# Kernel tuning notes

Hardware: AMD Instinct MI355X
Metric: run time of the kernel (lower is better)

## Reference

```python
import jax, jax.numpy as jnp
import numpy as np

N = 50000      # nodes
E = 800000     # edges (before self loops)
G = 64         # graphs in batch
F_IN = 11
HID = 64
C = 8
NEG_SLOPE = 0.2


def setup_inputs() -> dict:
    key = jax.random.key(0)
    ks = jax.random.split(key, 20)
    inp = {
        "x": jax.random.normal(ks[0], (N, F_IN), dtype=jnp.float32),
        "edge_index": jax.random.randint(ks[1], (2, E), 0, N, dtype=jnp.int64),
        "edge_attr": jax.random.normal(ks[2], (E, 17), dtype=jnp.float32),
        "batch": jnp.sort(jax.random.randint(ks[3], (N,), 0, G, dtype=jnp.int64)),
    }
    def glorot(k, shape):
        fan_in, fan_out = shape[0], shape[-1]
        s = jnp.sqrt(6.0 / (fan_in + fan_out))
        return jax.random.uniform(k, shape, jnp.float32, -s, s)
    # GATConv layers (heads=1): W [in,out], att vectors a_src/a_dst [out], bias [out]
    inp["W1"] = glorot(ks[4], (F_IN, HID)); inp["a1s"] = glorot(ks[5], (HID,)); inp["a1d"] = glorot(ks[6], (HID,)); inp["b1"] = jnp.zeros((HID,), jnp.float32)
    inp["W2"] = glorot(ks[7], (HID, HID)); inp["a2s"] = glorot(ks[8], (HID,)); inp["a2d"] = glorot(ks[9], (HID,)); inp["b2"] = jnp.zeros((HID,), jnp.float32)
    inp["W3"] = glorot(ks[10], (HID, C)); inp["a3s"] = glorot(ks[11], (C,)); inp["a3d"] = glorot(ks[12], (C,)); inp["b3"] = jnp.zeros((C,), jnp.float32)
    return inp


def _gat_layer(x, src, dst, W, a_s, a_d, b):
    # x: [N,in] -> h: [N,out]; single head, concat irrelevant for heads=1
    h = x @ W
    alpha_src = h @ a_s            # [N]
    alpha_dst = h @ a_d            # [N]
    e = jax.nn.leaky_relu(alpha_src[src] + alpha_dst[dst], negative_slope=NEG_SLOPE)  # [E']
    # segment-wise (per destination node) softmax over incoming edges
    m = jax.ops.segment_max(e, dst, num_segments=N)
    ex = jnp.exp(e - m[dst])
    denom = jax.ops.segment_sum(ex, dst, num_segments=N)
    alpha = ex / denom[dst]
    out = jax.ops.segment_sum(alpha[:, None] * h[src], dst, num_segments=N)
    return out + b


def reference(x, edge_index, edge_attr, batch, W1, a1s, a1d, b1, W2, a2s, a2d, b2, W3, a3s, a3d, b3):
    del edge_attr  # GATConv without edge_dim ignores edge_attr
    loop = jnp.arange(N, dtype=edge_index.dtype)
    src = jnp.concatenate([edge_index[0], loop])  # add self loops
    dst = jnp.concatenate([edge_index[1], loop])
    h = jax.nn.relu(_gat_layer(x, src, dst, W1, a1s, a1d, b1))
    h = jax.nn.relu(_gat_layer(h, src, dst, W2, a2s, a2d, b2))
    h = jax.nn.relu(_gat_layer(h, src, dst, W3, a3s, a3d, b3))
    # global mean pool over graphs
    counts = jax.ops.segment_sum(jnp.ones((N,), h.dtype), batch, num_segments=G)
    pooled = jax.ops.segment_sum(h, batch, num_segments=G) / jnp.maximum(counts, 1.0)[:, None]
    # dropout is identity in eval mode
    return jax.nn.sigmoid(pooled)
```

## Files before the change

kernel.cpp:

```cpp
#include <hip/hip_runtime.h>

#define NN 50000
#define EE 800000
#define GG 64
#define CC 8

#define NBKT 196
#define NCHK 782
#define CHUNK 1024
#define CAP 8192

__device__ unsigned g_done = 0;

__device__ __forceinline__ float lrelu(float z) { return fmaxf(z, 0.2f * z); }
__device__ __forceinline__ unsigned short f2bf(float v) {
    unsigned u = __float_as_uint(v);
    return (unsigned short)((u + 0x7FFFu + ((u >> 16) & 1u)) >> 16);
}
__device__ __forceinline__ float bf2f(unsigned short b) {
    return __uint_as_float(((unsigned)b) << 16);
}


__global__ __launch_bounds__(256) void k0_mm11_hist(const float* __restrict__ x, const float* __restrict__ W,
                                                    const float* __restrict__ avs, const float* __restrict__ avd,
                                                    unsigned short* __restrict__ h, float* __restrict__ as_,
                                                    float* __restrict__ ad_, const int* __restrict__ dst,
                                                    int* __restrict__ G) {
    __shared__ float xT[11 * 68];
    __shared__ float Wl[11 * 64];
    __shared__ float avl[64], adl[64];
    __shared__ int hist[NBKT];
    int t = threadIdx.x;
    int nbase = blockIdx.x * 64;
    for (int idx = t; idx < 11 * 64; idx += 256) Wl[idx] = W[idx];
    if (t < 64) { avl[t] = avs[t]; adl[t] = avd[t]; }
    for (int idx = t; idx < 64 * 11; idx += 256) {
        int n = idx / 11, k = idx - n * 11;
        int gn = nbase + n;
        if (gn >= NN) gn = NN - 1;
        xT[k * 68 + n] = x[gn * 11 + k];
    }
    for (int i = t; i < NBKT; i += 256) hist[i] = 0;
    __syncthreads();
    int f0 = (t & 15) * 4;
    int n0 = (t >> 4) * 4;
    float a00=0,a01=0,a02=0,a03=0, a10=0,a11=0,a12=0,a13=0;
    float a20=0,a21=0,a22=0,a23=0, a30=0,a31=0,a32=0,a33=0;
#pragma unroll
    for (int k = 0; k < 11; k++) {
        float4 xv = *(const float4*)&xT[k * 68 + n0];
        float4 wv = *(const float4*)&Wl[k * 64 + f0];
        a00 += xv.x * wv.x; a01 += xv.x * wv.y; a02 += xv.x * wv.z; a03 += xv.x * wv.w;
        a10 += xv.y * wv.x; a11 += xv.y * wv.y; a12 += xv.y * wv.z; a13 += xv.y * wv.w;
        a20 += xv.z * wv.x; a21 += xv.z * wv.y; a22 += xv.z * wv.z; a23 += xv.z * wv.w;
        a30 += xv.w * wv.x; a31 += xv.w * wv.y; a32 += xv.w * wv.z; a33 += xv.w * wv.w;
    }
    float4 av = *(const float4*)&avl[f0];
    float4 dv = *(const float4*)&adl[f0];
    float vs[4], vd[4];
    vs[0] = a00*av.x + a01*av.y + a02*av.z + a03*av.w;
    vs[1] = a10*av.x + a11*av.y + a12*av.z + a13*av.w;
    vs[2] = a20*av.x + a21*av.y + a22*av.z + a23*av.w;
    vs[3] = a30*av.x + a31*av.y + a32*av.z + a33*av.w;
    vd[0] = a00*dv.x + a01*dv.y + a02*dv.z + a03*dv.w;
    vd[1] = a10*dv.x + a11*dv.y + a12*dv.z + a13*dv.w;
    vd[2] = a20*dv.x + a21*dv.y + a22*dv.z + a23*dv.w;
    vd[3] = a30*dv.x + a31*dv.y + a32*dv.z + a33*dv.w;
#pragma unroll
    for (int o = 1; o < 16; o <<= 1) {
#pragma unroll
        for (int ni = 0; ni < 4; ni++) {
            vs[ni] += __shfl_xor(vs[ni], o);
            vd[ni] += __shfl_xor(vd[ni], o);
        }
    }
    ushort4* h4 = (ushort4*)h;
    int nn0 = nbase + n0;
    float rows[4][4] = {{a00,a01,a02,a03},{a10,a11,a12,a13},{a20,a21,a22,a23},{a30,a31,a32,a33}};
#pragma unroll
    for (int ni = 0; ni < 4; ni++) {
        if (nn0 + ni < NN) {
            ushort4 pv;
            pv.x = f2bf(rows[ni][0]); pv.y = f2bf(rows[ni][1]);
            pv.z = f2bf(rows[ni][2]); pv.w = f2bf(rows[ni][3]);
            h4[(nn0 + ni) * 16 + (t & 15)] = pv;
            if ((t & 15) == 0) { as_[nn0 + ni] = vs[ni]; ad_[nn0 + ni] = vd[ni]; }
        }
    }
    int e0 = blockIdx.x * CHUNK;
    int e1 = min(e0 + CHUNK, EE);
    for (int e = e0 + t; e < e1; e += 256) atomicAdd(&hist[dst[e] >> 8], 1);
    __syncthreads();
    for (int i = t; i < NBKT; i += 256) G[blockIdx.x * NBKT + i] = hist[i];
}


__global__ __launch_bounds__(256) void k1_scan(const int* __restrict__ G, int* __restrict__ offs,
                                               int* __restrict__ bT, float* __restrict__ pool,
                                               float* __restrict__ cntf, int* __restrict__ rowptr) {
    __shared__ int s[256];
    int t = threadIdx.x, j = blockIdx.x;
    int c0 = t * 4;
    int v0 = (c0 + 0 < NCHK) ? G[(c0 + 0) * NBKT + j] : 0;
    int v1 = (c0 + 1 < NCHK) ? G[(c0 + 1) * NBKT + j] : 0;
    int v2 = (c0 + 2 < NCHK) ? G[(c0 + 2) * NBKT + j] : 0;
    int v3 = (c0 + 3 < NCHK) ? G[(c0 + 3) * NBKT + j] : 0;
    int tsum = v0 + v1 + v2 + v3;
    s[t] = tsum;
    __syncthreads();
#pragma unroll
    for (int off = 1; off < 256; off <<= 1) {
        int u = (t >= off) ? s[t - off] : 0;
        __syncthreads();
        s[t] += u;
        __syncthreads();
    }
    int excl = s[t] - tsum;
    if (c0 + 0 < NCHK) offs[(c0 + 0) * NBKT + j] = excl;
    if (c0 + 1 < NCHK) offs[(c0 + 1) * NBKT + j] = excl + v0;
    if (c0 + 2 < NCHK) offs[(c0 + 2) * NBKT + j] = excl + v0 + v1;
    if (c0 + 3 < NCHK) offs[(c0 + 3) * NBKT + j] = excl + v0 + v1 + v2;
    if (t == 255) bT[j] = s[255];
    if (j == 0) {
        for (int i = t; i < GG * CC; i += 256) pool[i] = 0.f;
        if (t < GG) cntf[t] = 0.f;
        if (t == 0) rowptr[NN] = EE;
    }
}


__global__ __launch_bounds__(256) void k2_part(const int* __restrict__ src, const int* __restrict__ dst,
                                               const int* __restrict__ offs, const int* __restrict__ bT,
                                               unsigned* __restrict__ pairs) {
    __shared__ int s[256];
    __shared__ int bst[NBKT];
    __shared__ int cur[NBKT];
    int t = threadIdx.x, c = blockIdx.x;
    int v = (t < NBKT) ? bT[t] : 0;
    s[t] = v;
    __syncthreads();
#pragma unroll
    for (int off = 1; off < 256; off <<= 1) {
        int u = (t >= off) ? s[t - off] : 0;
        __syncthreads();
        s[t] += u;
        __syncthreads();
    }
    if (t < NBKT) bst[t] = s[t] - v;
    __syncthreads();
    for (int i = t; i < NBKT; i += 256) cur[i] = bst[i] + offs[c * NBKT + i];
    __syncthreads();
    int e0 = c * CHUNK, e1 = min(e0 + CHUNK, EE);
    for (int e = e0 + t; e < e1; e += 256) {
        int d = dst[e];
        int pos = atomicAdd(&cur[d >> 8], 1);
        pairs[pos] = (unsigned)src[e] | ((unsigned)(d & 255) << 16);
    }
}


__global__ __launch_bounds__(256) void k3_sort(const unsigned* __restrict__ pairs, const int* __restrict__ bT,
                                               int* __restrict__ col, int* __restrict__ rowptr) {
    __shared__ unsigned pL[CAP];
    __shared__ int hist[256];
    __shared__ int sc[256];
    int t = threadIdx.x, j = blockIdx.x;
    int v = (t < NBKT) ? bT[t] : 0;
    hist[t] = v;
    __syncthreads();
#pragma unroll
    for (int off = 1; off < 256; off <<= 1) {
        int u = (t >= off) ? hist[t - off] : 0;
        __syncthreads();
        hist[t] += u;
        __syncthreads();
    }
    if (t == j) { sc[0] = hist[t] - v; sc[1] = v; }
    __syncthreads();
    int start = sc[0];
    int cnt = sc[1];
    if (cnt > CAP) cnt = CAP;
    int nb = j * 256;
    int nodeCnt = min(256, NN - nb);
    __syncthreads();
    hist[t] = 0;
    __syncthreads();
    for (int i = t; i < cnt; i += 256) {
        unsigned p = pairs[start + i];
        pL[i] = p;
        atomicAdd(&hist[p >> 16], 1);
    }
    __syncthreads();
    int c2 = hist[t];
    sc[t] = c2;
    __syncthreads();
#pragma unroll
    for (int off = 1; off < 256; off <<= 1) {
        int u = (t >= off) ? sc[t - off] : 0;
        __syncthreads();
        sc[t] += u;
        __syncthreads();
    }
    int excl = sc[t] - c2;
    if (t < nodeCnt) rowptr[nb + t] = start + excl;
    hist[t] = excl;
    __syncthreads();
    for (int i = t; i < cnt; i += 256) {
        unsigned p = pL[i];
        int pos = atomicAdd(&hist[p >> 16], 1);
        col[start + pos] = (int)(p & 0xFFFFu);
    }
}


__global__ __launch_bounds__(256) void k_mm64t(const float* __restrict__ x, const float* __restrict__ W,
                                               const float* __restrict__ avs, const float* __restrict__ avd,
                                               unsigned short* __restrict__ h, float* __restrict__ as_,
                                               float* __restrict__ ad_) {
    __shared__ float xT[64 * 68];
    __shared__ float Wl[64 * 64];
    __shared__ float avl[64], adl[64];
    int t = threadIdx.x;
    int nbase = blockIdx.x * 64;
    for (int idx = t; idx < 64 * 64; idx += 256) Wl[idx] = W[idx];
    if (t < 64) { avl[t] = avs[t]; adl[t] = avd[t]; }
    for (int idx = t; idx < 64 * 64; idx += 256) {
        int n = idx / 64, k = idx - n * 64;
        int gn = nbase + n;
        if (gn >= NN) gn = NN - 1;
        xT[k * 68 + n] = x[gn * 64 + k];
    }
    __syncthreads();
    int f0 = (t & 15) * 4;
    int n0 = (t >> 4) * 4;
    float a00=0,a01=0,a02=0,a03=0, a10=0,a11=0,a12=0,a13=0;
    float a20=0,a21=0,a22=0,a23=0, a30=0,a31=0,a32=0,a33=0;
#pragma unroll 4
    for (int k = 0; k < 64; k++) {
        float4 xv = *(const float4*)&xT[k * 68 + n0];
        float4 wv = *(const float4*)&Wl[k * 64 + f0];
        a00 += xv.x * wv.x; a01 += xv.x * wv.y; a02 += xv.x * wv.z; a03 += xv.x * wv.w;
        a10 += xv.y * wv.x; a11 += xv.y * wv.y; a12 += xv.y * wv.z; a13 += xv.y * wv.w;
        a20 += xv.z * wv.x; a21 += xv.z * wv.y; a22 += xv.z * wv.z; a23 += xv.z * wv.w;
        a30 += xv.w * wv.x; a31 += xv.w * wv.y; a32 += xv.w * wv.z; a33 += xv.w * wv.w;
    }
    float4 av = *(const float4*)&avl[f0];
    float4 dv = *(const float4*)&adl[f0];
    float vs[4], vd[4];
    vs[0] = a00*av.x + a01*av.y + a02*av.z + a03*av.w;
    vs[1] = a10*av.x + a11*av.y + a12*av.z + a13*av.w;
    vs[2] = a20*av.x + a21*av.y + a22*av.z + a23*av.w;
    vs[3] = a30*av.x + a31*av.y + a32*av.z + a33*av.w;
    vd[0] = a00*dv.x + a01*dv.y + a02*dv.z + a03*dv.w;
    vd[1] = a10*dv.x + a11*dv.y + a12*dv.z + a13*dv.w;
    vd[2] = a20*dv.x + a21*dv.y + a22*dv.z + a23*dv.w;
    vd[3] = a30*dv.x + a31*dv.y + a32*dv.z + a33*dv.w;
#pragma unroll
    for (int o = 1; o < 16; o <<= 1) {
#pragma unroll
        for (int ni = 0; ni < 4; ni++) {
            vs[ni] += __shfl_xor(vs[ni], o);
            vd[ni] += __shfl_xor(vd[ni], o);
        }
    }
    ushort4* h4 = (ushort4*)h;
    int nn0 = nbase + n0;
    float rows[4][4] = {{a00,a01,a02,a03},{a10,a11,a12,a13},{a20,a21,a22,a23},{a30,a31,a32,a33}};
#pragma unroll
    for (int ni = 0; ni < 4; ni++) {
        if (nn0 + ni < NN) {
            ushort4 pv;
            pv.x = f2bf(rows[ni][0]); pv.y = f2bf(rows[ni][1]);
            pv.z = f2bf(rows[ni][2]); pv.w = f2bf(rows[ni][3]);
            h4[(nn0 + ni) * 16 + (t & 15)] = pv;
            if ((t & 15) == 0) { as_[nn0 + ni] = vs[ni]; ad_[nn0 + ni] = vd[ni]; }
        }
    }
}


__global__ __launch_bounds__(256) void k_mm8(const float* __restrict__ x, const float* __restrict__ W,
                                             const float* __restrict__ avs, const float* __restrict__ avd,
                                             unsigned short* __restrict__ h3, float* __restrict__ as_,
                                             float* __restrict__ ad_) {
    __shared__ float Wl[512];
    for (int idx = threadIdx.x; idx < 512; idx += 256) Wl[idx] = W[idx];
    __syncthreads();
    int node = blockIdx.x * 4 + (threadIdx.x >> 6);
    int lane = threadIdx.x & 63;
    if (node >= NN) return;
    int f = lane & 7, kc = lane >> 3;
    float xv = x[node * 64 + lane];
    float acc = 0.f;
#pragma unroll
    for (int j = 0; j < 8; j++) {
        int k = kc * 8 + j;
        acc += __shfl(xv, k) * Wl[k * 8 + f];
    }
    acc += __shfl_xor(acc, 8);
    acc += __shfl_xor(acc, 16);
    acc += __shfl_xor(acc, 32);
    if (lane < 8) h3[node * 8 + lane] = f2bf(acc);
    float vs = 0.f, vd = 0.f;
    if (lane < 8) {
        vs = acc * avs[lane];
        vd = acc * avd[lane];
    }
    vs += __shfl_xor(vs, 1); vs += __shfl_xor(vs, 2); vs += __shfl_xor(vs, 4);
    vd += __shfl_xor(vd, 1); vd += __shfl_xor(vd, 2); vd += __shfl_xor(vd, 4);
    if (lane == 0) {
        as_[node] = vs;
        ad_[node] = vd;
    }
}


__global__ __launch_bounds__(256) void k_agg64(const unsigned short* __restrict__ h,
                                               const int* __restrict__ rowptr,
                                               const int* __restrict__ col, const float* __restrict__ as_,
                                               const float* __restrict__ ad_, const float* __restrict__ bias,
                                               float* __restrict__ out) {
    __shared__ uint2 ws[4][64];
    int wid = threadIdx.x >> 6;
    int node = blockIdx.x * 4 + wid;
    int lane = threadIdx.x & 63;
    int rp0 = rowptr[node];
    int deg = rowptr[node + 1] - rp0;
    float adn = ad_[node];
    float zself = lrelu(as_[node] + adn);
    const ushort4* hb = (const ushort4*)h;
    int f = lane & 15, eg = lane >> 4;
    float4 acc = make_float4(0.f, 0.f, 0.f, 0.f);
    if (deg <= 64) {
        int s = 0;
        float z = -1e30f;
        if (lane < deg) {
            s = col[rp0 + lane];
            z = lrelu(as_[s] + adn);
        }
        float M = z;
#pragma unroll
        for (int o = 32; o; o >>= 1) M = fmaxf(M, __shfl_xor(M, o));
        M = fmaxf(M, zself);
        float ex = (lane < deg) ? __expf(z - M) : 0.f;
        float exs = __expf(zself - M);
        float sum = ex;
#pragma unroll
        for (int o = 32; o; o >>= 1) sum += __shfl_xor(sum, o);
        float inv = 1.f / (sum + exs);
        float wl = ex * inv;
        ws[wid][lane] = make_uint2(__float_as_uint(wl), (unsigned)s);
        __syncthreads();
        const uint4* wsp = (const uint4*)&ws[wid][0];
        for (int base = 0; base < deg; base += 8) {
            uint4 p = wsp[(base >> 1) + eg];
            float wa = __uint_as_float(p.x);
            float wb = __uint_as_float(p.z);
            ushort4 ha = hb[p.y * 16 + f];
            ushort4 hc = hb[p.w * 16 + f];
            acc.x += wa * bf2f(ha.x) + wb * bf2f(hc.x);
            acc.y += wa * bf2f(ha.y) + wb * bf2f(hc.y);
            acc.z += wa * bf2f(ha.z) + wb * bf2f(hc.z);
            acc.w += wa * bf2f(ha.w) + wb * bf2f(hc.w);
        }
        if (eg == 0) {
            float w0 = exs * inv;
            ushort4 hv = hb[node * 16 + f];
            acc.x += w0 * bf2f(hv.x);
            acc.y += w0 * bf2f(hv.y);
            acc.z += w0 * bf2f(hv.z);
            acc.w += w0 * bf2f(hv.w);
        }
    } else {
        __syncthreads();
        float m = -1e30f, l = 0.f;
        for (int i = lane; i < deg; i += 64) {
            float z = lrelu(as_[col[rp0 + i]] + adn);
            float mn = fmaxf(m, z);
            l = l * __expf(m - mn) + __expf(z - mn);
            m = mn;
        }
        if (lane == 0) {
            float mn = fmaxf(m, zself);
            l = l * __expf(m - mn) + __expf(zself - mn);
            m = mn;
        }
#pragma unroll
        for (int o = 32; o; o >>= 1) {
            float mo = __shfl_xor(m, o), lo = __shfl_xor(l, o);
            float mn = fmaxf(m, mo);
            l = l * __expf(m - mn) + lo * __expf(mo - mn);
            m = mn;
        }
        float Em = m;
        float inv = 1.f / l;
        for (int base = 0; base < deg; base += 4) {
            int i = base + eg;
            if (i < deg) {
                int sv = col[rp0 + i];
                float al = __expf(lrelu(as_[sv] + adn) - Em) * inv;
                ushort4 hv = hb[sv * 16 + f];
                acc.x += al * bf2f(hv.x);
                acc.y += al * bf2f(hv.y);
                acc.z += al * bf2f(hv.z);
                acc.w += al * bf2f(hv.w);
            }
        }
        if (eg == 0) {
            float al = __expf(zself - Em) * inv;
            ushort4 hv = hb[node * 16 + f];
            acc.x += al * bf2f(hv.x);
            acc.y += al * bf2f(hv.y);
            acc.z += al * bf2f(hv.z);
            acc.w += al * bf2f(hv.w);
        }
    }
#pragma unroll
    for (int o = 16; o <= 32; o <<= 1) {
        acc.x += __shfl_xor(acc.x, o);
        acc.y += __shfl_xor(acc.y, o);
        acc.z += __shfl_xor(acc.z, o);
        acc.w += __shfl_xor(acc.w, o);
    }
    if (eg == 0) {
        float4 bv = ((const float4*)bias)[f];
        float4 o4;
        o4.x = fmaxf(acc.x + bv.x, 0.f);
        o4.y = fmaxf(acc.y + bv.y, 0.f);
        o4.z = fmaxf(acc.z + bv.z, 0.f);
        o4.w = fmaxf(acc.w + bv.w, 0.f);
        ((float4*)out)[node * 16 + f] = o4;
    }
}

__global__ __launch_bounds__(256) void k_agg8(const unsigned short* __restrict__ h,
                                              const int* __restrict__ rowptr,
                                              const int* __restrict__ col, const float* __restrict__ as_,
                                              const float* __restrict__ ad_, const float* __restrict__ bias,
                                              float* __restrict__ out) {
    __shared__ uint2 ws[4][64];
    int wid = threadIdx.x >> 6;
    int node = blockIdx.x * 4 + wid;
    int lane = threadIdx.x & 63;
    int rp0 = rowptr[node];
    int deg = rowptr[node + 1] - rp0;
    float adn = ad_[node];
    float zself = lrelu(as_[node] + adn);
    const ushort2* h2v = (const ushort2*)h;
    int f = lane & 3, eg = lane >> 2;
    float2 acc = make_float2(0.f, 0.f);
    if (deg <= 64) {
        int s = 0;
        float z = -1e30f;
        if (lane < deg) {
            s = col[rp0 + lane];
            z = lrelu(as_[s] + adn);
        }
        float M = z;
#pragma unroll
        for (int o = 32; o; o >>= 1) M = fmaxf(M, __shfl_xor(M, o));
        M = fmaxf(M, zself);
        float ex = (lane < deg) ? __expf(z - M) : 0.f;
        float exs = __expf(zself - M);
        float sum = ex;
#pragma unroll
        for (int o = 32; o; o >>= 1) sum += __shfl_xor(sum, o);
        float inv = 1.f / (sum + exs);
        float wl = ex * inv;
        ws[wid][lane] = make_uint2(__float_as_uint(wl), (unsigned)s);
        __syncthreads();
        const uint4* wsp = (const uint4*)&ws[wid][0];
        for (int base = 0; base < deg; base += 32) {
            uint4 p = wsp[(base >> 1) + eg];
            float wa = __uint_as_float(p.x);
            float wb = __uint_as_float(p.z);
            ushort2 ha = h2v[p.y * 4 + f];
            ushort2 hc = h2v[p.w * 4 + f];
            acc.x += wa * bf2f(ha.x) + wb * bf2f(hc.x);
            acc.y += wa * bf2f(ha.y) + wb * bf2f(hc.y);
        }
        if (eg == 0) {
            float w0 = exs * inv;
            ushort2 hv = h2v[node * 4 + f];
            acc.x += w0 * bf2f(hv.x);
            acc.y += w0 * bf2f(hv.y);
        }
    } else {
        __syncthreads();
        float m = -1e30f, l = 0.f;
        for (int i = lane; i < deg; i += 64) {
            float z = lrelu(as_[col[rp0 + i]] + adn);
            float mn = fmaxf(m, z);
            l = l * __expf(m - mn) + __expf(z - mn);
            m = mn;
        }
        if (lane == 0) {
            float mn = fmaxf(m, zself);
            l = l * __expf(m - mn) + __expf(zself - mn);
            m = mn;
        }
#pragma unroll
        for (int o = 32; o; o >>= 1) {
            float mo = __shfl_xor(m, o), lo = __shfl_xor(l, o);
            float mn = fmaxf(m, mo);
            l = l * __expf(m - mn) + lo * __expf(mo - mn);
            m = mn;
        }
        float Em = m;
        float inv = 1.f / l;
        for (int base = 0; base < deg; base += 16) {
            int i = base + eg;
            if (i < deg) {
                int sv = col[rp0 + i];
                float al = __expf(lrelu(as_[sv] + adn) - Em) * inv;
                ushort2 hv = h2v[sv * 4 + f];
                acc.x += al * bf2f(hv.x);
                acc.y += al * bf2f(hv.y);
            }
        }
        if (eg == 0) {
            float al = __expf(zself - Em) * inv;
            ushort2 hv = h2v[node * 4 + f];
            acc.x += al * bf2f(hv.x);
            acc.y += al * bf2f(hv.y);
        }
    }
#pragma unroll
    for (int o = 4; o <= 32; o <<= 1) {
        acc.x += __shfl_xor(acc.x, o);
        acc.y += __shfl_xor(acc.y, o);
    }
    if (eg == 0) {
        float2 bv = ((const float2*)bias)[f];
        float2 o2;
        o2.x = fmaxf(acc.x + bv.x, 0.f);
        o2.y = fmaxf(acc.y + bv.y, 0.f);
        ((float2*)out)[node * 4 + f] = o2;
    }
}


__global__ __launch_bounds__(256) void k9_poolfinal(const float* __restrict__ h3, const int* __restrict__ batch,
                                                    float* __restrict__ pool, float* __restrict__ cntf,
                                                    float* __restrict__ out) {
    __shared__ float pl[GG * CC + GG];
    __shared__ int lastFlag;
    int t = threadIdx.x;
    for (int idx = t; idx < GG * CC + GG; idx += 256) pl[idx] = 0.f;
    __syncthreads();
    int node = blockIdx.x * 256 + t;
    if (node < NN) {
        int g = batch[node];
#pragma unroll
        for (int c = 0; c < CC; c++) atomicAdd(&pl[g * CC + c], h3[node * CC + c]);
        atomicAdd(&pl[GG * CC + g], 1.0f);
    }
    __syncthreads();
    for (int idx = t; idx < GG * CC + GG; idx += 256) {
        float v = pl[idx];
        if (idx < GG * CC)
            atomicAdd(&pool[idx], v);
        else
            atomicAdd(&cntf[idx - GG * CC], v);
    }
    __syncthreads();
    if (t == 0) {
        __threadfence();
        unsigned r = __hip_atomic_fetch_add(&g_done, 1u, __ATOMIC_ACQ_REL, __HIP_MEMORY_SCOPE_AGENT);
        lastFlag = (r == (unsigned)(NBKT - 1));
    }
    __syncthreads();
    if (lastFlag) {
        __threadfence();
        for (int i = t; i < GG * CC; i += 256) {
            int g = i >> 3;
            float c = __hip_atomic_load(&cntf[g], __ATOMIC_RELAXED, __HIP_MEMORY_SCOPE_AGENT);
            float p = __hip_atomic_load(&pool[i], __ATOMIC_RELAXED, __HIP_MEMORY_SCOPE_AGENT);
            float v = p / fmaxf(c, 1.0f);
            out[i] = 1.0f / (1.0f + __expf(-v));
        }
        if (t == 0)
            __hip_atomic_store(&g_done, 0u, __ATOMIC_RELAXED, __HIP_MEMORY_SCOPE_AGENT);
    }
}


extern "C" void kernel_launch(void* const* d_in, const int* in_sizes, int n_in,
                              void* d_out, int out_size, void* d_ws, size_t ws_size,
                              hipStream_t stream) {
    const float* x   = (const float*)d_in[0];
    const int*   ei  = (const int*)d_in[1];
    const int*   bat = (const int*)d_in[3];
    const float* W1  = (const float*)d_in[4];
    const float* a1s = (const float*)d_in[5];
    const float* a1d = (const float*)d_in[6];
    const float* b1  = (const float*)d_in[7];
    const float* W2  = (const float*)d_in[8];
    const float* a2s = (const float*)d_in[9];
    const float* a2d = (const float*)d_in[10];
    const float* b2  = (const float*)d_in[11];
    const float* W3  = (const float*)d_in[12];
    const float* a3s = (const float*)d_in[13];
    const float* a3d = (const float*)d_in[14];
    const float* b3  = (const float*)d_in[15];
    float* out = (float*)d_out;

    float* fb = (float*)d_ws;
    unsigned short* hA16 = (unsigned short*)fb;
    float* hB   = fb + NN * 32;
    unsigned short* h316 = (unsigned short*)(hB + NN * 64);
    float* h3b  = hB + NN * 64 + NN * 4;
    float* as_  = h3b + NN * 8;
    float* ad_  = as_ + NN;
    int* rowptr = (int*)(ad_ + NN);
    int* col    = rowptr + NN + 1;
    int* G      = col + EE;
    int* offs   = G + NCHK * NBKT;
    int* bT     = offs + NCHK * NBKT;
    unsigned* pairs = (unsigned*)(bT + 256);
    float* pool = (float*)(pairs + EE);
    float* cntf = pool + GG * CC;

    const int NB4  = (NN + 3) / 4;
    const int NB64 = (NN + 63) / 64;

    const int* srcE = ei;
    const int* dstE = ei + EE;

    k0_mm11_hist<<<NB64, 256, 0, stream>>>(x, W1, a1s, a1d, hA16, as_, ad_, dstE, G);
    k1_scan<<<NBKT, 256, 0, stream>>>(G, offs, bT, pool, cntf, rowptr);
    k2_part<<<NCHK, 256, 0, stream>>>(srcE, dstE, offs, bT, pairs);
    k3_sort<<<NBKT, 256, 0, stream>>>(pairs, bT, col, rowptr);

    k_agg64<<<NB4, 256, 0, stream>>>(hA16, rowptr, col, as_, ad_, b1, hB);
    k_mm64t<<<NB64, 256, 0, stream>>>(hB, W2, a2s, a2d, hA16, as_, ad_);
    k_agg64<<<NB4, 256, 0, stream>>>(hA16, rowptr, col, as_, ad_, b2, hB);
    k_mm8<<<NB4, 256, 0, stream>>>(hB, W3, a3s, a3d, h316, as_, ad_);
    k_agg8<<<NB4, 256, 0, stream>>>(h316, rowptr, col, as_, ad_, b3, h3b);
    k9_poolfinal<<<NBKT, 256, 0, stream>>>(h3b, bat, pool, cntf, out);
}
```

Before: 276.6 us.

## Fuse layer-3 matmul into layer-2 aggregation and pooling into layer-3 aggregation

The layer-3 projection (64->8) and its attention logits are now computed in the epilogue of the second 64-wide aggregation, using a padded shared copy of W3, so the separate k_mm8 kernel and its fp32 intermediate go away. Mean pooling is folded into the 8-wide aggregation through shared-memory atomics and a last-block finalize, which removes k9_poolfinal and the h3 round trip. The layer-1 aggregation output is stored as bf16 instead of fp32, halving that traffic but adding rounding error. As a cost, each 4-node block now flushes pooled partials with global atomics, and there are many more such blocks than before.

New measurement: 651.7 us. +135.6%, slower.

```diff
diff --git a/kernel.cpp b/kernel.cpp
--- a/kernel.cpp
+++ b/kernel.cpp
@@ -9,6 +9,7 @@
 #define NCHK 782
 #define CHUNK 1024
 #define CAP 8192
+#define NB4G 12500
 
 __device__ unsigned g_done = 0;
 
@@ -214,7 +215,8 @@
 }
 
 
-__global__ __launch_bounds__(256) void k_mm64t(const float* __restrict__ x, const float* __restrict__ W,
+__global__ __launch_bounds__(256) void k_mm64t(const unsigned short* __restrict__ xin,
+                                               const float* __restrict__ W,
                                                const float* __restrict__ avs, const float* __restrict__ avd,
                                                unsigned short* __restrict__ h, float* __restrict__ as_,
                                                float* __restrict__ ad_) {
@@ -229,7 +231,7 @@
         int n = idx / 64, k = idx - n * 64;
         int gn = nbase + n;
         if (gn >= NN) gn = NN - 1;
-        xT[k * 68 + n] = x[gn * 64 + k];
+        xT[k * 68 + n] = bf2f(xin[gn * 64 + k]);
     }
     __syncthreads();
     int f0 = (t & 15) * 4;
@@ -280,48 +282,21 @@
 }
 
 
-__global__ __launch_bounds__(256) void k_mm8(const float* __restrict__ x, const float* __restrict__ W,
-                                             const float* __restrict__ avs, const float* __restrict__ avd,
-                                             unsigned short* __restrict__ h3, float* __restrict__ as_,
-                                             float* __restrict__ ad_) {
-    __shared__ float Wl[512];
-    for (int idx = threadIdx.x; idx < 512; idx += 256) Wl[idx] = W[idx];
-    __syncthreads();
-    int node = blockIdx.x * 4 + (threadIdx.x >> 6);
-    int lane = threadIdx.x & 63;
-    if (node >= NN) return;
-    int f = lane & 7, kc = lane >> 3;
-    float xv = x[node * 64 + lane];
-    float acc = 0.f;
-#pragma unroll
-    for (int j = 0; j < 8; j++) {
-        int k = kc * 8 + j;
-        acc += __shfl(xv, k) * Wl[k * 8 + f];
-    }
-    acc += __shfl_xor(acc, 8);
-    acc += __shfl_xor(acc, 16);
-    acc += __shfl_xor(acc, 32);
-    if (lane < 8) h3[node * 8 + lane] = f2bf(acc);
-    float vs = 0.f, vd = 0.f;
-    if (lane < 8) {
-        vs = acc * avs[lane];
-        vd = acc * avd[lane];
-    }
-    vs += __shfl_xor(vs, 1); vs += __shfl_xor(vs, 2); vs += __shfl_xor(vs, 4);
-    vd += __shfl_xor(vd, 1); vd += __shfl_xor(vd, 2); vd += __shfl_xor(vd, 4);
-    if (lane == 0) {
-        as_[node] = vs;
-        ad_[node] = vd;
-    }
-}
-
-
+template <bool FUSE>
 __global__ __launch_bounds__(256) void k_agg64(const unsigned short* __restrict__ h,
                                                const int* __restrict__ rowptr,
                                                const int* __restrict__ col, const float* __restrict__ as_,
                                                const float* __restrict__ ad_, const float* __restrict__ bias,
-                                               float* __restrict__ out) {
+                                               unsigned short* __restrict__ out16,
+                                               const float* __restrict__ W3, const float* __restrict__ a3s,
+                                               const float* __restrict__ a3d,
+                                               float* __restrict__ as3, float* __restrict__ ad3) {
     __shared__ uint2 ws[4][64];
+    __shared__ float W3p[64 * 10];
+    if constexpr (FUSE) {
+        for (int idx = threadIdx.x; idx < 512; idx += 256)
+            W3p[(idx >> 3) * 10 + (idx & 7)] = W3[idx];
+    }
     int wid = threadIdx.x >> 6;
     int node = blockIdx.x * 4 + wid;
     int lane = threadIdx.x & 63;
@@ -423,26 +398,63 @@
         acc.z += __shfl_xor(acc.z, o);
         acc.w += __shfl_xor(acc.w, o);
     }
-    if (eg == 0) {
-        float4 bv = ((const float4*)bias)[f];
-        float4 o4;
-        o4.x = fmaxf(acc.x + bv.x, 0.f);
-        o4.y = fmaxf(acc.y + bv.y, 0.f);
-        o4.z = fmaxf(acc.z + bv.z, 0.f);
-        o4.w = fmaxf(acc.w + bv.w, 0.f);
-        ((float4*)out)[node * 16 + f] = o4;
-    }
-}
-
-__global__ __launch_bounds__(256) void k_agg8(const unsigned short* __restrict__ h,
-                                              const int* __restrict__ rowptr,
-                                              const int* __restrict__ col, const float* __restrict__ as_,
-                                              const float* __restrict__ ad_, const float* __restrict__ bias,
-                                              float* __restrict__ out) {
+    float4 bv = ((const float4*)bias)[f];
+    float r0 = fmaxf(acc.x + bv.x, 0.f);
+    float r1 = fmaxf(acc.y + bv.y, 0.f);
+    float r2 = fmaxf(acc.z + bv.z, 0.f);
+    float r3 = fmaxf(acc.w + bv.w, 0.f);
+    if constexpr (!FUSE) {
+        if (eg == 0) {
+            ushort4 pv;
+            pv.x = f2bf(r0); pv.y = f2bf(r1); pv.z = f2bf(r2); pv.w = f2bf(r3);
+            ((ushort4*)out16)[node * 16 + f] = pv;
+        }
+    } else {
+        int j0 = eg * 2;
+        int kb = f * 4;
+        float p0 = 0.f, p1 = 0.f;
+#pragma unroll
+        for (int i = 0; i < 4; i++) {
+            float2 w = *(const float2*)&W3p[(kb + i) * 10 + j0];
+            float rv = (i == 0) ? r0 : (i == 1) ? r1 : (i == 2) ? r2 : r3;
+            p0 += rv * w.x;
+            p1 += rv * w.y;
+        }
+#pragma unroll
+        for (int o = 1; o < 16; o <<= 1) {
+            p0 += __shfl_xor(p0, o);
+            p1 += __shfl_xor(p1, o);
+        }
+        float vs = p0 * a3s[j0] + p1 * a3s[j0 + 1];
+        float vd = p0 * a3d[j0] + p1 * a3d[j0 + 1];
+        vs += __shfl_xor(vs, 16); vs += __shfl_xor(vs, 32);
+        vd += __shfl_xor(vd, 16); vd += __shfl_xor(vd, 32);
+        if (lane == 0) { as3[node] = vs; ad3[node] = vd; }
+        if (f == 0) {
+            ushort2 pv;
+            pv.x = f2bf(p0); pv.y = f2bf(p1);
+            ((ushort2*)out16)[node * 4 + eg] = pv;
+        }
+    }
+}
+
+
+__global__ __launch_bounds__(256) void k_agg8pool(const unsigned short* __restrict__ h,
+                                                  const int* __restrict__ rowptr,
+                                                  const int* __restrict__ col, const float* __restrict__ as_,
+                                                  const float* __restrict__ ad_, const float* __restrict__ bias,
+                                                  const int* __restrict__ batch, float* __restrict__ pool,
+                                                  float* __restrict__ cntf, float* __restrict__ out) {
     __shared__ uint2 ws[4][64];
-    int wid = threadIdx.x >> 6;
+    __shared__ float plB[GG * CC];
+    __shared__ float plC[GG];
+    __shared__ int lastFlag;
+    int t = threadIdx.x;
+    for (int i = t; i < GG * CC; i += 256) plB[i] = 0.f;
+    if (t < GG) plC[t] = 0.f;
+    int wid = t >> 6;
     int node = blockIdx.x * 4 + wid;
-    int lane = threadIdx.x & 63;
+    int lane = t & 63;
     int rp0 = rowptr[node];
     int deg = rowptr[node + 1] - rp0;
     float adn = ad_[node];
@@ -531,44 +543,32 @@
         acc.x += __shfl_xor(acc.x, o);
         acc.y += __shfl_xor(acc.y, o);
     }
-    if (eg == 0) {
-        float2 bv = ((const float2*)bias)[f];
-        float2 o2;
-        o2.x = fmaxf(acc.x + bv.x, 0.f);
-        o2.y = fmaxf(acc.y + bv.y, 0.f);
-        ((float2*)out)[node * 4 + f] = o2;
-    }
-}
-
-
-__global__ __launch_bounds__(256) void k9_poolfinal(const float* __restrict__ h3, const int* __restrict__ batch,
-                                                    float* __restrict__ pool, float* __restrict__ cntf,
-                                                    float* __restrict__ out) {
-    __shared__ float pl[GG * CC + GG];
-    __shared__ int lastFlag;
-    int t = threadIdx.x;
-    for (int idx = t; idx < GG * CC + GG; idx += 256) pl[idx] = 0.f;
-    __syncthreads();
-    int node = blockIdx.x * 256 + t;
-    if (node < NN) {
-        int g = batch[node];
-#pragma unroll
-        for (int c = 0; c < CC; c++) atomicAdd(&pl[g * CC + c], h3[node * CC + c]);
-        atomicAdd(&pl[GG * CC + g], 1.0f);
-    }
-    __syncthreads();
-    for (int idx = t; idx < GG * CC + GG; idx += 256) {
-        float v = pl[idx];
-        if (idx < GG * CC)
-            atomicAdd(&pool[idx], v);
-        else
-            atomicAdd(&cntf[idx - GG * CC], v);
+    {
+        float2 bvv = ((const float2*)bias)[f];
+        float o0 = fmaxf(acc.x + bvv.x, 0.f);
+        float o1 = fmaxf(acc.y + bvv.y, 0.f);
+        if (eg == 0) {
+            int g = batch[node];
+            atomicAdd(&plB[g * CC + 2 * f], o0);
+            atomicAdd(&plB[g * CC + 2 * f + 1], o1);
+            if (f == 0) atomicAdd(&plC[g], 1.0f);
+        }
+    }
+    __syncthreads();
+    for (int i = t; i < GG * CC + GG; i += 256) {
+        if (i < GG * CC) {
+            float v = plB[i];
+            if (v != 0.f) atomicAdd(&pool[i], v);
+        } else {
+            float v = plC[i - GG * CC];
+            if (v != 0.f) atomicAdd(&cntf[i - GG * CC], v);
+        }
     }
     __syncthreads();
     if (t == 0) {
         __threadfence();
         unsigned r = __hip_atomic_fetch_add(&g_done, 1u, __ATOMIC_ACQ_REL, __HIP_MEMORY_SCOPE_AGENT);
-        lastFlag = (r == (unsigned)(NBKT - 1));
+        lastFlag = (r == (unsigned)(NB4G - 1));
     }
     __syncthreads();
     if (lastFlag) {
@@ -608,12 +608,13 @@
 
     float* fb = (float*)d_ws;
     unsigned short* hA16 = (unsigned short*)fb;
-    float* hB   = fb + NN * 32;
-    unsigned short* h316 = (unsigned short*)(hB + NN * 64);
-    float* h3b  = hB + NN * 64 + NN * 4;
-    float* as_  = h3b + NN * 8;
+    unsigned short* hB16 = (unsigned short*)(fb + NN * 32);
+    unsigned short* h316 = (unsigned short*)(fb + NN * 64);
+    float* as_  = fb + NN * 64 + NN * 4;
     float* ad_  = as_ + NN;
-    int* rowptr = (int*)(ad_ + NN);
+    float* as3  = ad_ + NN;
+    float* ad3  = as3 + NN;
+    int* rowptr = (int*)(ad3 + NN);
     int* col    = rowptr + NN + 1;
     int* G      = col + EE;
     int* offs   = G + NCHK * NBKT;
@@ -622,7 +623,6 @@
     float* pool = (float*)(pairs + EE);
     float* cntf = pool + GG * CC;
 
-    const int NB4  = (NN + 3) / 4;
     const int NB64 = (NN + 63) / 64;
 
     const int* srcE = ei;
@@ -633,10 +633,10 @@
     k2_part<<<NCHK, 256, 0, stream>>>(srcE, dstE, offs, bT, pairs);
     k3_sort<<<NBKT, 256, 0, stream>>>(pairs, bT, col, rowptr);
 
-    k_agg64<<<NB4, 256, 0, stream>>>(hA16, rowptr, col, as_, ad_, b1, hB);
-    k_mm64t<<<NB64, 256, 0, stream>>>(hB, W2, a2s, a2d, hA16, as_, ad_);
-    k_agg64<<<NB4, 256, 0, stream>>>(hA16, rowptr, col, as_, ad_, b2, hB);
-    k_mm8<<<NB4, 256, 0, stream>>>(hB, W3, a3s, a3d, h316, as_, ad_);
-    k_agg8<<<NB4, 256, 0, stream>>>(h316, rowptr, col, as_, ad_, b3, h3b);
-    k9_poolfinal<<<NBKT, 256, 0, stream>>>(h3b, bat, pool, cntf, out);
-}
+    k_agg64<false><<<NB4G, 256, 0, stream>>>(hA16, rowptr, col, as_, ad_, b1, hB16,
+                                             nullptr, nullptr, nullptr, nullptr, nullptr);
+    k_mm64t<<<NB64, 256, 0, stream>>>(hB16, W2, a2s, a2d, hA16, as_, ad_);
+    k_agg64<true><<<NB4G, 256, 0, stream>>>(hA16, rowptr, col, as_, ad_, b2, h316,
+                                            W3, a3s, a3d, as3, ad3);
+    k_agg8pool<<<NB4G, 256, 0, stream>>>(h316, rowptr, col, as3, ad3, b3, bat, pool, cntf, out);
+}
```
